# Optimization experiments

Measured on AMD Instinct MI355X. Metric: run time of the kernel, lower is better.

The kernel has to match this reference:

```python
import jax, jax.numpy as jnp
import numpy as np

N, D = 8192, 128


def setup_inputs() -> dict:
    key = jax.random.key(0)
    k1, k2 = jax.random.split(key)
    emb = jax.random.normal(k1, (N, D), dtype=jnp.float32)
    graphWeight = jax.random.uniform(k2, (N, N), dtype=jnp.float32)
    return {"emb": emb, "graphWeight": graphWeight}


def _pairwise_l2(x):
    # cdist(x, x, p=2) via the ||a-b||^2 = ||a||^2 + ||b||^2 - 2 a.b identity.
    sq_norms = jnp.sum(x * x, axis=-1)  # [N]
    sq = sq_norms[:, None] + sq_norms[None, :] - 2.0 * (x @ x.T)  # [N, N]
    sq = jnp.maximum(sq, 0.0)
    # safe sqrt (grad-safe at exactly-zero distances, e.g. the diagonal)
    return jnp.where(sq > 0.0, jnp.sqrt(jnp.where(sq > 0.0, sq, 1.0)), 0.0)


def reference(emb, graphWeight):
    dist = _pairwise_l2(emb)                 # [N, N]
    dist = dist / jnp.max(dist)              # normalize by global max
    return jnp.mean((1.0 - dist) * graphWeight)  # scalar loss
```

## Files before the change

kernel.cpp:

```cpp
#include <hip/hip_runtime.h>
#include <hip/hip_bf16.h>

#define NN 8192
#define DD 128
#define JT 16
#define JR 16

typedef __attribute__((ext_vector_type(8))) short short8;
typedef __attribute__((ext_vector_type(4))) float f32x4;

__device__ __forceinline__ unsigned short f2bf(float x) {
    unsigned u = __float_as_uint(x);
    u += 0x7FFFu + ((u >> 16) & 1u);
    return (unsigned short)(u >> 16);
}
__device__ __forceinline__ float bf2f(unsigned short b) {
    return __uint_as_float(((unsigned)b) << 16);
}

__device__ __forceinline__ void gld_lds16(const float* src, float* ldst) {
    __builtin_amdgcn_global_load_lds(
        (const __attribute__((address_space(1))) void*)src,
        (__attribute__((address_space(3))) void*)ldst, 16, 0, 0);
}

__global__ void prep_kernel(const float* __restrict__ emb,
                            unsigned short* __restrict__ ebf,
                            float* __restrict__ nrm) {
    int row  = blockIdx.x * 4 + (threadIdx.x >> 6);
    int lane = threadIdx.x & 63;
    const float2 v = *reinterpret_cast<const float2*>(emb + (size_t)row * DD + lane * 2);
    unsigned short b0 = f2bf(v.x), b1 = f2bf(v.y);
    ushort2 st; st.x = b0; st.y = b1;
    *reinterpret_cast<ushort2*>(ebf + (size_t)row * DD + lane * 2) = st;
    float f0 = bf2f(b0), f1 = bf2f(b1);
    float s = f0 * f0 + f1 * f1;
    #pragma unroll
    for (int m = 32; m; m >>= 1) s += __shfl_xor(s, m);
    if (lane == 0) nrm[row] = s;
}

__global__ __launch_bounds__(256, 3)
void gram_kernel(const unsigned short* __restrict__ ebf,
                 const float* __restrict__ nrm,
                 const float* __restrict__ W,
                 float4* __restrict__ part) {
    __shared__ float wlds[4][3][JR * 32];
    __shared__ float sw_s[4], sdw_s[4], dm_s[4];

    const int wave = threadIdx.x >> 6;
    const int lane = threadIdx.x & 63;
    const int lr = lane & 15;
    const int hi = lane >> 4;

    const int i0w = blockIdx.x * 128 + wave * 32;
    const int j0  = blockIdx.y * 256;

    const int srow = lane >> 3;
    const int schk = (lane & 7) ^ srow;
    const float* wsrc = W + (size_t)(j0 + srow) * NN + i0w + schk * 4;

    short8 af[4][2];
    #pragma unroll
    for (int kc = 0; kc < 4; ++kc)
        #pragma unroll
        for (int m = 0; m < 2; ++m)
            af[kc][m] = *reinterpret_cast<const short8*>(
                ebf + (size_t)(i0w + m * 16 + lr) * DD + kc * 32 + hi * 8);
    f32x4 ni4[2];
    #pragma unroll
    for (int m = 0; m < 2; ++m)
        ni4[m] = *reinterpret_cast<const f32x4*>(nrm + i0w + m * 16 + hi * 4);

    auto stage = [&](int t, int buf) {
        float* dst = &wlds[wave][buf][0];
        const float* s = wsrc + (size_t)t * JR * NN;
        gld_lds16(s, dst);
        gld_lds16(s + 8 * NN, dst + 256);
    };
    auto loadbf = [&](int t, short8 (&bf)[4], float& nj) {
        const int jr = j0 + t * JR + lr;
        #pragma unroll
        for (int kc = 0; kc < 4; ++kc)
            bf[kc] = *reinterpret_cast<const short8*>(
                ebf + (size_t)jr * DD + kc * 32 + hi * 8);
        nj = nrm[jr];
    };

    short8 bfA[4], bfB[4];
    float njA = 0.f, njB = 0.f;
    float sW = 0.f, sDW = 0.f, dmax = 0.f;

    stage(0, 0);
    __builtin_amdgcn_sched_barrier(0);
    loadbf(0, bfA, njA);
    __builtin_amdgcn_sched_barrier(0);
    stage(1, 1);
    __builtin_amdgcn_sched_barrier(0);

    auto doTile = [&](int t, short8 (&bfc)[4], float& njc,
                      short8 (&bfn)[4], float& njn) {
        if (t < JT - 1) asm volatile("s_waitcnt vmcnt(2)" ::: "memory");
        else            asm volatile("s_waitcnt vmcnt(0)" ::: "memory");
        __builtin_amdgcn_sched_barrier(0);

        const float* lb = &wlds[wave][t % 3][0];
        f32x4 w4[2];
        #pragma unroll
        for (int m = 0; m < 2; ++m)
            w4[m] = *reinterpret_cast<const f32x4*>(
                lb + lr * 32 + (((m * 4 + hi) ^ (lr & 7)) * 4));
        __builtin_amdgcn_sched_barrier(0);

        f32x4 acc[2] = {(f32x4){0.f,0.f,0.f,0.f}, (f32x4){0.f,0.f,0.f,0.f}};
        #pragma unroll
        for (int kc = 0; kc < 4; ++kc)
            #pragma unroll
            for (int m = 0; m < 2; ++m)
                acc[m] = __builtin_amdgcn_mfma_f32_16x16x32_bf16(
                    af[kc][m], bfc[kc], acc[m], 0, 0, 0);

        if (t + 1 < JT) loadbf(t + 1, bfn, njn);
        __builtin_amdgcn_sched_barrier(0);
        if (t + 2 < JT) stage(t + 2, (t + 2) % 3);
        __builtin_amdgcn_sched_barrier(0);

        #pragma unroll
        for (int m = 0; m < 2; ++m)
            #pragma unroll
            for (int r = 0; r < 4; ++r) {
                float sq = ni4[m][r] + njc - 2.0f * acc[m][r];
                float d = sqrtf(fmaxf(sq, 0.0f));
                sW  += w4[m][r];
                sDW += w4[m][r] * d;
                dmax = fmaxf(dmax, d);
            }
    };

    #pragma unroll
    for (int t = 0; t < JT; t += 2) {
        doTile(t,     bfA, njA, bfB, njB);
        doTile(t + 1, bfB, njB, bfA, njA);
    }

    #pragma unroll
    for (int m = 32; m; m >>= 1) {
        sW  += __shfl_xor(sW, m);
        sDW += __shfl_xor(sDW, m);
        dmax = fmaxf(dmax, __shfl_xor(dmax, m));
    }
    if (lane == 0) { sw_s[wave] = sW; sdw_s[wave] = sDW; dm_s[wave] = dmax; }
    __syncthreads();
    if (threadIdx.x == 0) {
        float SW = 0.f, SDW = 0.f, DM = 0.f;
        #pragma unroll
        for (int k = 0; k < 4; ++k) {
            SW += sw_s[k]; SDW += sdw_s[k]; DM = fmaxf(DM, dm_s[k]);
        }
        float4 p; p.x = SW; p.y = SDW; p.z = DM; p.w = 0.f;
        part[blockIdx.y * gridDim.x + blockIdx.x] = p;
    }
}

__global__ __launch_bounds__(512)
void reduce_kernel(const float4* __restrict__ part, int nblk,
                   float* __restrict__ out) {
    const int tid = threadIdx.x;
    double sW = 0.0, sDW = 0.0;
    float dmax = 0.f;
    for (int idx = tid; idx < nblk; idx += 512) {
        float4 p = part[idx];
        sW += (double)p.x; sDW += (double)p.y; dmax = fmaxf(dmax, p.z);
    }
    #pragma unroll
    for (int m = 32; m; m >>= 1) {
        sW  += __shfl_xor(sW, m);
        sDW += __shfl_xor(sDW, m);
        dmax = fmaxf(dmax, __shfl_xor(dmax, m));
    }
    __shared__ double sw_s[8], sdw_s[8];
    __shared__ float dm_s[8];
    const int w = tid >> 6, l = tid & 63;
    if (l == 0) { sw_s[w] = sW; sdw_s[w] = sDW; dm_s[w] = dmax; }
    __syncthreads();
    if (tid == 0) {
        double SW = 0.0, SDW = 0.0; float DM = 0.f;
        #pragma unroll
        for (int k = 0; k < 8; ++k) {
            SW += sw_s[k]; SDW += sdw_s[k]; DM = fmaxf(DM, dm_s[k]);
        }
        out[0] = (float)((SW - SDW / (double)DM) / ((double)NN * (double)NN));
    }
}

extern "C" void kernel_launch(void* const* d_in, const int* in_sizes, int n_in,
                              void* d_out, int out_size, void* d_ws, size_t ws_size,
                              hipStream_t stream) {
    const float* emb = (const float*)d_in[0];
    const float* W   = (const float*)d_in[1];
    float* out = (float*)d_out;

    char* ws = (char*)d_ws;
    float4* part        = (float4*)ws;
    unsigned short* ebf = (unsigned short*)(ws + 65536);
    float* nrm          = (float*)(ws + 65536 + (size_t)NN * DD * 2);

    prep_kernel<<<NN / 4, 256, 0, stream>>>(emb, ebf, nrm);
    dim3 grid(NN / 128, NN / 256);
    gram_kernel<<<grid, 256, 0, stream>>>(ebf, nrm, W, part);
    reduce_kernel<<<1, 512, 0, stream>>>(part, grid.x * grid.y, out);
}
```

Baseline: 89.27 us.

## Deepen gram kernel pipeline to four stages with longer per-block J range

Each block now walks 64 tiles of 16 j-rows instead of 16, which cuts the grid by four and shrinks the partial buffer. The W staging ring grows from three to four LDS buffers per wave, with hand-written ds_read_b128 using immediate offsets, precomputed pointers and explicit vmcnt waits, so three tiles of W and B fragments stay in flight. The goal is to hide more of the HBM latency on the 256MB W stream. In exchange, occupancy drops to 2 blocks per CU, register pressure rises from four B fragment sets, and there are fewer blocks to balance across CUs.

New measurement: 85.23 us. -4.5%, faster.

```diff
diff --git a/kernel.cpp b/kernel.cpp
--- a/kernel.cpp
+++ b/kernel.cpp
@@ -3,11 +3,11 @@
 
 #define NN 8192
 #define DD 128
-#define JT 16
-#define JR 16
+#define JT 64
 
 typedef __attribute__((ext_vector_type(8))) short short8;
 typedef __attribute__((ext_vector_type(4))) float f32x4;
+typedef __attribute__((address_space(3))) float lds_f;
 
 __device__ __forceinline__ unsigned short f2bf(float x) {
     unsigned u = __float_as_uint(x);
@@ -40,12 +40,71 @@
     if (lane == 0) nrm[row] = s;
 }
 
-__global__ __launch_bounds__(256, 3)
+#define DO_TILE(NSTR, ISSUE, OFFS, SOFF, bfc, njc, bff, njf)                   \
+  {                                                                            \
+    asm volatile("s_waitcnt vmcnt(" NSTR ")" ::: "memory");                    \
+    __builtin_amdgcn_sched_barrier(0);                                         \
+    f32x4 w40, w41;                                                            \
+    asm volatile("ds_read_b128 %0, %2 offset:" OFFS "\n\t"                     \
+                 "ds_read_b128 %1, %3 offset:" OFFS                            \
+                 : "=&v"(w40), "=&v"(w41)                                      \
+                 : "v"(lp0), "v"(lp1));                                        \
+    __builtin_amdgcn_sched_barrier(0);                                         \
+    if (ISSUE) {                                                               \
+      bff[0] = *reinterpret_cast<const short8*>(ebnext);                       \
+      bff[1] = *reinterpret_cast<const short8*>(ebnext + 32);                  \
+      bff[2] = *reinterpret_cast<const short8*>(ebnext + 64);                  \
+      bff[3] = *reinterpret_cast<const short8*>(ebnext + 96);                  \
+      njf = *njnext;                                                           \
+      __builtin_amdgcn_sched_barrier(0);                                       \
+      gld_lds16(wnext,          sbase + (SOFF));                               \
+      gld_lds16(wnext + 8 * NN, sbase + (SOFF) + 256);                         \
+      ebnext += 16 * DD; njnext += 16; wnext += (size_t)16 * NN;               \
+    }                                                                          \
+    __builtin_amdgcn_sched_barrier(0);                                         \
+    f32x4 a0 = {0.f,0.f,0.f,0.f}, a1 = {0.f,0.f,0.f,0.f};                      \
+    a0 = __builtin_amdgcn_mfma_f32_16x16x32_bf16(af[0][0], bfc[0], a0,0,0,0);  \
+    a1 = __builtin_amdgcn_mfma_f32_16x16x32_bf16(af[0][1], bfc[0], a1,0,0,0);  \
+    a0 = __builtin_amdgcn_mfma_f32_16x16x32_bf16(af[1][0], bfc[1], a0,0,0,0);  \
+    a1 = __builtin_amdgcn_mfma_f32_16x16x32_bf16(af[1][1], bfc[1], a1,0,0,0);  \
+    a0 = __builtin_amdgcn_mfma_f32_16x16x32_bf16(af[2][0], bfc[2], a0,0,0,0);  \
+    a1 = __builtin_amdgcn_mfma_f32_16x16x32_bf16(af[2][1], bfc[2], a1,0,0,0);  \
+    a0 = __builtin_amdgcn_mfma_f32_16x16x32_bf16(af[3][0], bfc[3], a0,0,0,0);  \
+    a1 = __builtin_amdgcn_mfma_f32_16x16x32_bf16(af[3][1], bfc[3], a1,0,0,0);  \
+    asm volatile("s_waitcnt lgkmcnt(0)" ::: "memory");                         \
+    __builtin_amdgcn_sched_barrier(0);                                         \
+    for (int r = 0; r < 4; ++r) {                                              \
+      float sq = ni4[0][r] + (njc) - 2.0f * a0[r];                             \
+      float d  = sqrtf(fmaxf(sq, 0.0f));                                       \
+      sW += w40[r]; sDW += w40[r] * d; dmax = fmaxf(dmax, d);                  \
+    }                                                                          \
+    for (int r = 0; r < 4; ++r) {                                              \
+      float sq = ni4[1][r] + (njc) - 2.0f * a1[r];                             \
+      float d  = sqrtf(fmaxf(sq, 0.0f));                                       \
+      sW += w41[r]; sDW += w41[r] * d; dmax = fmaxf(dmax, d);                  \
+    }                                                                          \
+  }
+
+#define PRO_PAIR(bff, njf, SOFF)                                               \
+  {                                                                            \
+    bff[0] = *reinterpret_cast<const short8*>(ebnext);                         \
+    bff[1] = *reinterpret_cast<const short8*>(ebnext + 32);                    \
+    bff[2] = *reinterpret_cast<const short8*>(ebnext + 64);                    \
+    bff[3] = *reinterpret_cast<const short8*>(ebnext + 96);                    \
+    njf = *njnext;                                                             \
+    __builtin_amdgcn_sched_barrier(0);                                         \
+    gld_lds16(wnext,          sbase + (SOFF));                                 \
+    gld_lds16(wnext + 8 * NN, sbase + (SOFF) + 256);                           \
+    ebnext += 16 * DD; njnext += 16; wnext += (size_t)16 * NN;                 \
+    __builtin_amdgcn_sched_barrier(0);                                         \
+  }
+
+__global__ __launch_bounds__(256, 2)
 void gram_kernel(const unsigned short* __restrict__ ebf,
                  const float* __restrict__ nrm,
                  const float* __restrict__ W,
                  float4* __restrict__ part) {
-    __shared__ float wlds[4][3][JR * 32];
+    __shared__ float wlds[4][4][16 * 32];
     __shared__ float sw_s[4], sdw_s[4], dm_s[4];
 
     const int wave = threadIdx.x >> 6;
@@ -54,11 +113,20 @@
     const int hi = lane >> 4;
 
     const int i0w = blockIdx.x * 128 + wave * 32;
-    const int j0  = blockIdx.y * 256;
+    const int j0  = blockIdx.y * (JT * 16);
 
     const int srow = lane >> 3;
     const int schk = (lane & 7) ^ srow;
-    const float* wsrc = W + (size_t)(j0 + srow) * NN + i0w + schk * 4;
+
+    const float* wnext = W + (size_t)(j0 + srow) * NN + i0w + schk * 4;
+    const unsigned short* ebnext = ebf + (size_t)(j0 + lr) * DD + hi * 8;
+    const float* njnext = nrm + j0 + lr;
+
+    float* sbase = &wlds[wave][0][0];
+    const int chunk0 = hi ^ (lr & 7);
+    const int chunk1 = (4 + hi) ^ (lr & 7);
+    const lds_f* lp0 = (const lds_f*)(sbase + lr * 32 + chunk0 * 4);
+    const lds_f* lp1 = (const lds_f*)(sbase + lr * 32 + chunk1 * 4);
 
     short8 af[4][2];
     #pragma unroll
@@ -71,77 +139,26 @@
     #pragma unroll
     for (int m = 0; m < 2; ++m)
         ni4[m] = *reinterpret_cast<const f32x4*>(nrm + i0w + m * 16 + hi * 4);
-
-    auto stage = [&](int t, int buf) {
-        float* dst = &wlds[wave][buf][0];
-        const float* s = wsrc + (size_t)t * JR * NN;
-        gld_lds16(s, dst);
-        gld_lds16(s + 8 * NN, dst + 256);
-    };
-    auto loadbf = [&](int t, short8 (&bf)[4], float& nj) {
-        const int jr = j0 + t * JR + lr;
-        #pragma unroll
-        for (int kc = 0; kc < 4; ++kc)
-            bf[kc] = *reinterpret_cast<const short8*>(
-                ebf + (size_t)jr * DD + kc * 32 + hi * 8);
-        nj = nrm[jr];
-    };
-
-    short8 bfA[4], bfB[4];
-    float njA = 0.f, njB = 0.f;
+    __builtin_amdgcn_sched_barrier(0);
+
+    short8 bfA[4], bfB[4], bfC[4], bfD[4];
+    float njA = 0.f, njB = 0.f, njC = 0.f, njD = 0.f;
     float sW = 0.f, sDW = 0.f, dmax = 0.f;
 
-    stage(0, 0);
-    __builtin_amdgcn_sched_barrier(0);
-    loadbf(0, bfA, njA);
-    __builtin_amdgcn_sched_barrier(0);
-    stage(1, 1);
-    __builtin_amdgcn_sched_barrier(0);
-
-    auto doTile = [&](int t, short8 (&bfc)[4], float& njc,
-                      short8 (&bfn)[4], float& njn) {
-        if (t < JT - 1) asm volatile("s_waitcnt vmcnt(2)" ::: "memory");
-        else            asm volatile("s_waitcnt vmcnt(0)" ::: "memory");
-        __builtin_amdgcn_sched_barrier(0);
-
-        const float* lb = &wlds[wave][t % 3][0];
-        f32x4 w4[2];
-        #pragma unroll
-        for (int m = 0; m < 2; ++m)
-            w4[m] = *reinterpret_cast<const f32x4*>(
-                lb + lr * 32 + (((m * 4 + hi) ^ (lr & 7)) * 4));
-        __builtin_amdgcn_sched_barrier(0);
-
-        f32x4 acc[2] = {(f32x4){0.f,0.f,0.f,0.f}, (f32x4){0.f,0.f,0.f,0.f}};
-        #pragma unroll
-        for (int kc = 0; kc < 4; ++kc)
-            #pragma unroll
-            for (int m = 0; m < 2; ++m)
-                acc[m] = __builtin_amdgcn_mfma_f32_16x16x32_bf16(
-                    af[kc][m], bfc[kc], acc[m], 0, 0, 0);
-
-        if (t + 1 < JT) loadbf(t + 1, bfn, njn);
-        __builtin_amdgcn_sched_barrier(0);
-        if (t + 2 < JT) stage(t + 2, (t + 2) % 3);
-        __builtin_amdgcn_sched_barrier(0);
-
-        #pragma unroll
-        for (int m = 0; m < 2; ++m)
-            #pragma unroll
-            for (int r = 0; r < 4; ++r) {
-                float sq = ni4[m][r] + njc - 2.0f * acc[m][r];
-                float d = sqrtf(fmaxf(sq, 0.0f));
-                sW  += w4[m][r];
-                sDW += w4[m][r] * d;
-                dmax = fmaxf(dmax, d);
-            }
-    };
-
-    #pragma unroll
-    for (int t = 0; t < JT; t += 2) {
-        doTile(t,     bfA, njA, bfB, njB);
-        doTile(t + 1, bfB, njB, bfA, njA);
-    }
+    PRO_PAIR(bfA, njA, 0);
+    PRO_PAIR(bfB, njB, 512);
+    PRO_PAIR(bfC, njC, 1024);
+
+    for (int t4 = 0; t4 < JT - 4; t4 += 4) {
+        DO_TILE("14", 1, "0",    1536, bfA, njA, bfD, njD);
+        DO_TILE("14", 1, "2048", 0,    bfB, njB, bfA, njA);
+        DO_TILE("14", 1, "4096", 512,  bfC, njC, bfB, njB);
+        DO_TILE("14", 1, "6144", 1024, bfD, njD, bfC, njC);
+    }
+    DO_TILE("14", 1, "0",    1536, bfA, njA, bfD, njD);
+    DO_TILE("14", 0, "2048", 0,    bfB, njB, bfA, njA);
+    DO_TILE("7",  0, "4096", 0,    bfC, njC, bfA, njA);
+    DO_TILE("0",  0, "6144", 0,    bfD, njD, bfA, njA);
 
     #pragma unroll
     for (int m = 32; m; m >>= 1) {
@@ -202,11 +219,11 @@
 
     char* ws = (char*)d_ws;
     float4* part        = (float4*)ws;
-    unsigned short* ebf = (unsigned short*)(ws + 65536);
-    float* nrm          = (float*)(ws + 65536 + (size_t)NN * DD * 2);
+    unsigned short* ebf = (unsigned short*)(ws + 16384);
+    float* nrm          = (float*)(ws + 16384 + (size_t)NN * DD * 2);
 
     prep_kernel<<<NN / 4, 256, 0, stream>>>(emb, ebf, nrm);
-    dim3 grid(NN / 128, NN / 256);
+    dim3 grid(NN / 128, NN / (JT * 16));
     gram_kernel<<<grid, 256, 0, stream>>>(ebf, nrm, W, part);
     reduce_kernel<<<1, 512, 0, stream>>>(part, grid.x * grid.y, out);
 }
```
